# Optimization experiments

Hardware: AMD Instinct MI355X
Metric: run time of the kernel (lower is better)

The kernel has to match this reference:

```python
import jax, jax.numpy as jnp
import numpy as np

N = 1024   # num nodes
D = 128    # feat_dim (input_dim)


def setup_inputs() -> dict:
    key = jax.random.key(0)
    k1, k2 = jax.random.split(key)
    x = jax.random.normal(k1, (N, D), dtype=jnp.float32)
    # nn.Linear(D, 1) -> weight vector [D], bias [1] (xavier init weight, zero bias)
    w_vec = jax.random.normal(k2, (D,), dtype=jnp.float32) * np.sqrt(2.0 / (D + 1))
    w_bias = jnp.zeros((1,), dtype=jnp.float32)
    return {"x": x, "w_vec": w_vec, "w_bias": w_bias}


def reference(x, w_vec, w_bias):
    # diff[i, j, d] = |x[i, d] - x[j, d]|  (repeat_interleave row-major -> x[i] minus broadcast x[j])
    diff = jnp.abs(x[:, None, :] - x[None, :, :])          # [N, N, D]
    scores = jnp.einsum('ijd,d->ij', diff, w_vec) + w_bias[0]  # Linear(D,1) -> [N, N]
    scores = jax.nn.relu(scores)
    return jax.nn.softmax(scores, axis=1)
```

## Files before the change

### kernel.cpp

```cpp
#include <hip/hip_runtime.h>

#define N 1024
#define D 128
#define PAD 132

__global__ __launch_bounds__(256) void scores_kernel(
    const float* __restrict__ x, const float* __restrict__ w,
    const float* __restrict__ bias, float* __restrict__ S) {
  __shared__ float sxi[64 * PAD];
  __shared__ float sxj[32 * PAD];

  const int t  = threadIdx.x;
  const int bi = blockIdx.y * 64;
  const int bj = blockIdx.x * 32;

  {
    const int c  = t & 31;
    const int r0 = t >> 5;
    #pragma unroll
    for (int p = 0; p < 8; ++p) {
      const int r = r0 + p * 8;
      const float4 v = reinterpret_cast<const float4*>(x)[(bi + r) * 32 + c];
      *reinterpret_cast<float4*>(&sxi[r * PAD + c * 4]) = v;
    }
    #pragma unroll
    for (int p = 0; p < 4; ++p) {
      const int r = r0 + p * 8;
      const float4 v = reinterpret_cast<const float4*>(x)[(bj + r) * 32 + c];
      *reinterpret_cast<float4*>(&sxj[r * PAD + c * 4]) = v;
    }
  }
  __syncthreads();

  const int tx = t & 15;
  const int ty = t >> 4;

  float acc[4][2];
  #pragma unroll
  for (int a = 0; a < 4; ++a)
    #pragma unroll
    for (int b = 0; b < 2; ++b) acc[a][b] = 0.f;

  #pragma unroll 4
  for (int d = 0; d < D; d += 4) {
    const float4 W = reinterpret_cast<const float4*>(w)[d >> 2];
    float4 A[4], B[2];
    #pragma unroll
    for (int a = 0; a < 4; ++a)
      A[a] = *reinterpret_cast<const float4*>(&sxi[(ty + 16 * a) * PAD + d]);
    #pragma unroll
    for (int b = 0; b < 2; ++b)
      B[b] = *reinterpret_cast<const float4*>(&sxj[(tx + 16 * b) * PAD + d]);

    #pragma unroll
    for (int a = 0; a < 4; ++a) {
      #pragma unroll
      for (int b = 0; b < 2; ++b) {
        float s = acc[a][b];
        s = fmaf(fabsf(A[a].x - B[b].x), W.x, s);
        s = fmaf(fabsf(A[a].y - B[b].y), W.y, s);
        s = fmaf(fabsf(A[a].z - B[b].z), W.z, s);
        s = fmaf(fabsf(A[a].w - B[b].w), W.w, s);
        acc[a][b] = s;
      }
    }
  }

  const float bv = bias[0];
  #pragma unroll
  for (int a = 0; a < 4; ++a) {
    const int row = bi + ty + 16 * a;
    #pragma unroll
    for (int b = 0; b < 2; ++b) {
      const int col = bj + tx + 16 * b;
      S[row * N + col] = fmaxf(acc[a][b] + bv, 0.f);
    }
  }
}

__global__ __launch_bounds__(256) void softmax_kernel(float* __restrict__ S) {
  __shared__ float sred[8];
  const int t = threadIdx.x;
  float4* rowp = reinterpret_cast<float4*>(S + blockIdx.x * N);
  float4 v = rowp[t];

  float m = fmaxf(fmaxf(v.x, v.y), fmaxf(v.z, v.w));
  #pragma unroll
  for (int o = 32; o > 0; o >>= 1) m = fmaxf(m, __shfl_xor(m, o, 64));
  if ((t & 63) == 0) sred[t >> 6] = m;
  __syncthreads();
  m = fmaxf(fmaxf(sred[0], sred[1]), fmaxf(sred[2], sred[3]));

  float4 e;
  e.x = __expf(v.x - m);
  e.y = __expf(v.y - m);
  e.z = __expf(v.z - m);
  e.w = __expf(v.w - m);
  float s = (e.x + e.y) + (e.z + e.w);
  #pragma unroll
  for (int o = 32; o > 0; o >>= 1) s += __shfl_xor(s, o, 64);
  if ((t & 63) == 0) sred[4 + (t >> 6)] = s;
  __syncthreads();
  s = (sred[4] + sred[5]) + (sred[6] + sred[7]);

  const float r = 1.0f / s;
  e.x *= r; e.y *= r; e.z *= r; e.w *= r;
  rowp[t] = e;
}

extern "C" void kernel_launch(void* const* d_in, const int* in_sizes, int n_in,
                              void* d_out, int out_size, void* d_ws, size_t ws_size,
                              hipStream_t stream) {
  const float* x  = (const float*)d_in[0];
  const float* w  = (const float*)d_in[1];
  const float* b  = (const float*)d_in[2];
  float* out = (float*)d_out;

  dim3 grid(N / 32, N / 64);
  scores_kernel<<<grid, 256, 0, stream>>>(x, w, b, out);
  softmax_kernel<<<N, 256, 0, stream>>>(out);
}
```

Before: 74.03 us.

## Fuse scores and softmax into one kernel with an atomic grid barrier

Merges the score kernel and the row-softmax kernel into a single launch using 64x64 tiles. Each block exponentiates its relu'd scores and atomically adds per-row partial sums into workspace, then waits at a spin-wait grid barrier before normalising and writing the output once. This removes the second launch and the extra write/read/write pass over the N×N score matrix. It drops the max subtraction, relying on relu'd scores staying small enough not to overflow exp. It also relies on all 256 blocks being co-resident. The flag is never reset across calls, so later calls can race with block (0,0)'s re-zeroing of rowsum and counter.

```diff
diff --git a/kernel.cpp b/kernel.cpp
--- a/kernel.cpp
+++ b/kernel.cpp
@@ -3,16 +3,37 @@
 #define N 1024
 #define D 128
 #define PAD 132
+#define MAGIC 0x3C96A5E1u
 
-__global__ __launch_bounds__(256) void scores_kernel(
+__global__ __launch_bounds__(256) void fused_kernel(
     const float* __restrict__ x, const float* __restrict__ w,
-    const float* __restrict__ bias, float* __restrict__ S) {
+    const float* __restrict__ bias, float* __restrict__ S,
+    unsigned int* __restrict__ ws) {
   __shared__ float sxi[64 * PAD];
-  __shared__ float sxj[32 * PAD];
+  __shared__ float sxj[64 * PAD];
+
+  unsigned int* flag    = ws;
+  unsigned int* counter = ws + 32;
+  float* rowsum = reinterpret_cast<float*>(ws) + 1024;
 
   const int t  = threadIdx.x;
   const int bi = blockIdx.y * 64;
-  const int bj = blockIdx.x * 32;
+  const int bj = blockIdx.x * 64;
+
+  if (blockIdx.x == 0 && blockIdx.y == 0) {
+    #pragma unroll
+    for (int k = 0; k < 4; ++k)
+      __hip_atomic_store(&rowsum[t * 4 + k], 0.0f, __ATOMIC_RELAXED,
+                         __HIP_MEMORY_SCOPE_AGENT);
+    if (t == 0)
+      __hip_atomic_store(counter, 0u, __ATOMIC_RELAXED,
+                         __HIP_MEMORY_SCOPE_AGENT);
+    __syncthreads();
+    __threadfence();
+    if (t == 0)
+      __hip_atomic_store(flag, MAGIC, __ATOMIC_RELEASE,
+                         __HIP_MEMORY_SCOPE_AGENT);
+  }
 
   {
     const int c  = t & 31;
@@ -20,14 +41,10 @@
     #pragma unroll
     for (int p = 0; p < 8; ++p) {
       const int r = r0 + p * 8;
-      const float4 v = reinterpret_cast<const float4*>(x)[(bi + r) * 32 + c];
-      *reinterpret_cast<float4*>(&sxi[r * PAD + c * 4]) = v;
-    }
-    #pragma unroll
-    for (int p = 0; p < 4; ++p) {
-      const int r = r0 + p * 8;
-      const float4 v = reinterpret_cast<const float4*>(x)[(bj + r) * 32 + c];
-      *reinterpret_cast<float4*>(&sxj[r * PAD + c * 4]) = v;
+      const float4 vi = reinterpret_cast<const float4*>(x)[(bi + r) * 32 + c];
+      *reinterpret_cast<float4*>(&sxi[r * PAD + c * 4]) = vi;
+      const float4 vj = reinterpret_cast<const float4*>(x)[(bj + r) * 32 + c];
+      *reinterpret_cast<float4*>(&sxj[r * PAD + c * 4]) = vj;
     }
   }
   __syncthreads();
@@ -35,27 +52,27 @@
   const int tx = t & 15;
   const int ty = t >> 4;
 
-  float acc[4][2];
+  float acc[4][4];
   #pragma unroll
   for (int a = 0; a < 4; ++a)
     #pragma unroll
-    for (int b = 0; b < 2; ++b) acc[a][b] = 0.f;
+    for (int b = 0; b < 4; ++b) acc[a][b] = 0.f;
 
-  #pragma unroll 4
+  #pragma unroll 2
   for (int d = 0; d < D; d += 4) {
     const float4 W = reinterpret_cast<const float4*>(w)[d >> 2];
-    float4 A[4], B[2];
+    float4 A[4], B[4];
     #pragma unroll
     for (int a = 0; a < 4; ++a)
       A[a] = *reinterpret_cast<const float4*>(&sxi[(ty + 16 * a) * PAD + d]);
     #pragma unroll
-    for (int b = 0; b < 2; ++b)
+    for (int b = 0; b < 4; ++b)
       B[b] = *reinterpret_cast<const float4*>(&sxj[(tx + 16 * b) * PAD + d]);
 
     #pragma unroll
     for (int a = 0; a < 4; ++a) {
       #pragma unroll
-      for (int b = 0; b < 2; ++b) {
+      for (int b = 0; b < 4; ++b) {
         float s = acc[a][b];
         s = fmaf(fabsf(A[a].x - B[b].x), W.x, s);
         s = fmaf(fabsf(A[a].y - B[b].y), W.y, s);
@@ -67,56 +84,74 @@
   }
 
   const float bv = bias[0];
+  float e[4][4];
+  float part[4];
+  #pragma unroll
+  for (int a = 0; a < 4; ++a) {
+    float p = 0.f;
+    #pragma unroll
+    for (int b = 0; b < 4; ++b) {
+      const float s  = fmaxf(acc[a][b] + bv, 0.f);
+      const float ev = __expf(s);
+      e[a][b] = ev;
+      p += ev;
+    }
+    #pragma unroll
+    for (int o = 1; o < 16; o <<= 1) p += __shfl_xor(p, o, 64);
+    part[a] = p;
+  }
+
+  if (t == 0) {
+    for (unsigned it = 0; it < (1u << 26); ++it) {
+      if (__hip_atomic_load(flag, __ATOMIC_ACQUIRE,
+                            __HIP_MEMORY_SCOPE_AGENT) == MAGIC) break;
+      __builtin_amdgcn_s_sleep(2);
+    }
+  }
+  __syncthreads();
+
+  if (tx == 0) {
+    #pragma unroll
+    for (int a = 0; a < 4; ++a)
+      atomicAdd(&rowsum[bi + ty + 16 * a], part[a]);
+  }
+  __syncthreads();
+
+  if (t == 0) {
+    __hip_atomic_fetch_add(counter, 1u, __ATOMIC_ACQ_REL,
+                           __HIP_MEMORY_SCOPE_AGENT);
+    for (unsigned it = 0; it < (1u << 26); ++it) {
+      if (__hip_atomic_load(counter, __ATOMIC_ACQUIRE,
+                            __HIP_MEMORY_SCOPE_AGENT) >= 256u) break;
+      __builtin_amdgcn_s_sleep(2);
+    }
+  }
+  __syncthreads();
+
+  float rs[4];
+  #pragma unroll
+  for (int a = 0; a < 4; ++a)
+    rs[a] = 1.0f / __hip_atomic_load(&rowsum[bi + ty + 16 * a],
+                                     __ATOMIC_RELAXED, __HIP_MEMORY_SCOPE_AGENT);
+
   #pragma unroll
   for (int a = 0; a < 4; ++a) {
     const int row = bi + ty + 16 * a;
     #pragma unroll
-    for (int b = 0; b < 2; ++b) {
-      const int col = bj + tx + 16 * b;
-      S[row * N + col] = fmaxf(acc[a][b] + bv, 0.f);
-    }
+    for (int b = 0; b < 4; ++b)
+      S[row * N + bj + tx + 16 * b] = e[a][b] * rs[a];
   }
-}
-
-__global__ __launch_bounds__(256) void softmax_kernel(float* __restrict__ S) {
-  __shared__ float sred[8];
-  const int t = threadIdx.x;
-  float4* rowp = reinterpret_cast<float4*>(S + blockIdx.x * N);
-  float4 v = rowp[t];
-
-  float m = fmaxf(fmaxf(v.x, v.y), fmaxf(v.z, v.w));
-  #pragma unroll
-  for (int o = 32; o > 0; o >>= 1) m = fmaxf(m, __shfl_xor(m, o, 64));
-  if ((t & 63) == 0) sred[t >> 6] = m;
-  __syncthreads();
-  m = fmaxf(fmaxf(sred[0], sred[1]), fmaxf(sred[2], sred[3]));
-
-  float4 e;
-  e.x = __expf(v.x - m);
-  e.y = __expf(v.y - m);
-  e.z = __expf(v.z - m);
-  e.w = __expf(v.w - m);
-  float s = (e.x + e.y) + (e.z + e.w);
-  #pragma unroll
-  for (int o = 32; o > 0; o >>= 1) s += __shfl_xor(s, o, 64);
-  if ((t & 63) == 0) sred[4 + (t >> 6)] = s;
-  __syncthreads();
-  s = (sred[4] + sred[5]) + (sred[6] + sred[7]);
-
-  const float r = 1.0f / s;
-  e.x *= r; e.y *= r; e.z *= r; e.w *= r;
-  rowp[t] = e;
 }
 
 extern "C" void kernel_launch(void* const* d_in, const int* in_sizes, int n_in,
                               void* d_out, int out_size, void* d_ws, size_t ws_size,
                               hipStream_t stream) {
-  const float* x  = (const float*)d_in[0];
-  const float* w  = (const float*)d_in[1];
-  const float* b  = (const float*)d_in[2];
+  const float* x = (const float*)d_in[0];
+  const float* w = (const float*)d_in[1];
+  const float* b = (const float*)d_in[2];
   float* out = (float*)d_out;
+  unsigned int* ws = (unsigned int*)d_ws;
 
-  dim3 grid(N / 32, N / 64);
-  scores_kernel<<<grid, 256, 0, stream>>>(x, w, b, out);
-  softmax_kernel<<<N, 256, 0, stream>>>(out);
+  dim3 grid(N / 64, N / 64);
+  fused_kernel<<<grid, 256, 0, stream>>>(x, w, b, out, ws);
 }
```

Result: slower. 83.40 us (+12.6%).
